# Optimization experiments

Measured on AMD Instinct MI355X. Metric: run time of the kernel, lower is better.

## Reference

```python
import jax, jax.numpy as jnp
import numpy as np

B, T, D_MODEL, STATE = 4, 4096, 1024, 256
LN_EPS = 1e-5


def setup_inputs() -> dict:
    key = jax.random.key(0)
    ks = jax.random.split(key, 8)
    x = jax.random.normal(ks[0], (B, T, D_MODEL), dtype=jnp.float32)
    bound_d = 1.0 / np.sqrt(D_MODEL)
    bound_n = 1.0 / np.sqrt(STATE)
    Wa_w = jax.random.normal(ks[1], (STATE, D_MODEL), dtype=jnp.float32) * 0.02
    Wa_b = jnp.zeros((STATE,), dtype=jnp.float32)
    WB_w = jax.random.normal(ks[2], (STATE, D_MODEL), dtype=jnp.float32) * 0.02
    WB_b = jax.random.uniform(ks[3], (STATE,), jnp.float32, -bound_d, bound_d)
    WC_w = jax.random.normal(ks[4], (D_MODEL, STATE), dtype=jnp.float32) * 0.02
    WC_b = jax.random.uniform(ks[5], (D_MODEL,), jnp.float32, -bound_n, bound_n)
    log_gamma = jnp.asarray(0.0, dtype=jnp.float32)
    D_skip = jax.random.normal(ks[6], (D_MODEL,), dtype=jnp.float32) * 0.01
    ln_w = jnp.ones((D_MODEL,), dtype=jnp.float32)
    ln_b = jnp.zeros((D_MODEL,), dtype=jnp.float32)
    return {"x": x, "Wa_w": Wa_w, "Wa_b": Wa_b, "log_gamma": log_gamma,
            "WB_w": WB_w, "WB_b": WB_b, "WC_w": WC_w, "WC_b": WC_b,
            "D_skip": D_skip, "ln_w": ln_w, "ln_b": ln_b}


def _layernorm(x, w, b):
    mu = jnp.mean(x, axis=-1, keepdims=True)
    var = jnp.mean(jnp.square(x - mu), axis=-1, keepdims=True)
    return (x - mu) * jax.lax.rsqrt(var + LN_EPS) * w + b


def reference(x, Wa_w, Wa_b, log_gamma, WB_w, WB_b, WC_w, WC_b, D_skip, ln_w, ln_b):
    residual = x
    xn = _layernorm(x, ln_w, ln_b)                      # (B,T,D)
    # Fourier eigenvalues: gamma * tanh(W_a x), FFT, magnitude-contracting scale
    gamma = jax.nn.sigmoid(log_gamma)
    a = gamma * jnp.tanh(jnp.einsum('btd,nd->btn', xn, Wa_w) + Wa_b)  # (B,T,n) real
    a_hat = jnp.fft.fft(a, axis=-1)                     # (B,T,n) complex, conj-symmetric
    mag = jnp.maximum(jnp.abs(a_hat), 1e-8)
    a_hat = a_hat * jax.nn.sigmoid(2.0 * (1.0 - mag))
    # Input projection in Fourier domain
    u = jnp.einsum('btd,nd->btn', xn, WB_w) + WB_b
    u_hat = jnp.fft.fft(u, axis=-1)                     # (B,T,n) complex
    # Linear recurrence h_t = a_t * h_{t-1} + b_t via associative scan over time
    def combine(c1, c2):
        a1, b1 = c1
        a2, b2 = c2
        return (a1 * a2, a2 * b1 + b2)
    _, h_hat = jax.lax.associative_scan(combine, (a_hat, u_hat), axis=1)
    h = jnp.real(jnp.fft.ifft(h_hat, axis=-1)).astype(x.dtype)        # (B,T,n)
    y = jnp.einsum('btn,dn->btd', h, WC_w) + WC_b + D_skip * residual
    return y
```

## Files before the change

### kernel.cpp

```cpp
#include <hip/hip_runtime.h>


typedef unsigned short ushort_t;
typedef short s16x8 __attribute__((ext_vector_type(8)));
typedef float f32x4 __attribute__((ext_vector_type(4)));
typedef _Float16 f16x8 __attribute__((ext_vector_type(8)));
typedef _Float16 f16x2 __attribute__((ext_vector_type(2)));

#define B_ 4
#define T_ 4096
#define D_ 1024
#define N_ 256
#define KB_ 129
#define M_ (B_*T_)

#define SWZ(i) ((i) ^ (((i) >> 3) & 6))
#define DR4(n) ((((n) & 3) << 6) | (((n) & 12) << 2) | (((n) & 48) >> 2) | (((n) >> 6) & 3))

__device__ __forceinline__ ushort_t f2bf(float f) {
  unsigned u = __float_as_uint(f);
  u = (u + 0x7FFFu + ((u >> 16) & 1u)) >> 16;
  return (ushort_t)u;
}
__device__ __forceinline__ float2 cmul(float2 a, float2 b) {
  return make_float2(a.x*b.x - a.y*b.y, a.x*b.y + a.y*b.x);
}
__device__ __forceinline__ float fast_tanh(float x) {
  return 1.f - 2.f / (__expf(2.f * x) + 1.f);
}

typedef const __attribute__((address_space(1))) unsigned glb_u32;
typedef __attribute__((address_space(3))) unsigned lds_u32;
__device__ __forceinline__ void gload16(const void* g, void* l) {
  __builtin_amdgcn_global_load_lds((glb_u32*)g, (lds_u32*)l, 16, 0, 0);
}

__global__ __launch_bounds__(256) void stats_prep_kernel(const float* __restrict__ x,
    float2* __restrict__ stats,
    const float* __restrict__ Wa, const float* __restrict__ WB,
    const float* __restrict__ WC, ushort_t* __restrict__ Wab,
    ushort_t* __restrict__ WCb) {
  int tid = threadIdx.x;
  if (blockIdx.x >= 4096) {
    int i4 = ((blockIdx.x - 4096) * 256 + tid) * 4;
    float4 v;
    ushort_t* dst;
    if (i4 < 262144)        { v = *(const float4*)(Wa + i4);          dst = Wab + i4; }
    else if (i4 < 524288)   { v = *(const float4*)(WB + i4 - 262144); dst = Wab + i4; }
    else                    { v = *(const float4*)(WC + i4 - 524288); dst = WCb + i4 - 524288; }
    ushort4 o;
    o.x = f2bf(v.x); o.y = f2bf(v.y); o.z = f2bf(v.z); o.w = f2bf(v.w);
    *(ushort4*)dst = o;
    return;
  }
  int lane = tid & 63, wv = tid >> 6;
  int row = blockIdx.x * 4 + wv;
  const float4* xr = (const float4*)(x + (size_t)row * D_);
  float s = 0.f, sq = 0.f;
  #pragma unroll
  for (int j = 0; j < 4; ++j) {
    float4 v = xr[lane + 64 * j];
    s  += v.x + v.y + v.z + v.w;
    sq += v.x*v.x + v.y*v.y + v.z*v.z + v.w*v.w;
  }
  #pragma unroll
  for (int off = 32; off >= 1; off >>= 1) {
    s  += __shfl_xor(s, off);
    sq += __shfl_xor(sq, off);
  }
  if (lane == 0) {
    float mu  = s * (1.0f / D_);
    float var = sq * (1.0f / D_) - mu * mu;
    stats[row] = make_float2(mu, rsqrtf(var + 1e-5f));
  }
}

__global__ __launch_bounds__(256) void gemm1_ln(
    const float* __restrict__ x, const float2* __restrict__ stats,
    const float* __restrict__ lnw, const float* __restrict__ lnb,
    const ushort_t* __restrict__ B, _Float16* __restrict__ C) {
  constexpr int NF = 2;
  __shared__ ushort_t Alds[128 * 64];
  __shared__ ushort_t Blds[64 * 64];
  int bid = blockIdx.x;
  int cpx = gridDim.x >> 3;
  bid = (bid & 7) * cpx + (bid >> 3);
  int mt = bid >> 3, nt = bid & 7;
  int m0 = mt * 128, n0 = nt * 64;
  int tid = threadIdx.x;
  int lane = tid & 63, wid = tid >> 6;
  int wm = wid >> 1, wn = wid & 1;

  int lr8 = lane >> 3;
  int gd  = (lane & 7) ^ lr8;
  const ushort_t* gB = B + (size_t)(n0 + wid * 16 + lr8) * D_ + gd * 8;
  ushort_t* lB = &Blds[(wid * 16) * 64];

  int rsub = tid >> 4, l16 = tid & 15;
  int slotA = ((l16 >> 1) ^ (rsub & 7)) * 8 + (l16 & 1) * 4;
  float2 st[8];
  #pragma unroll
  for (int it = 0; it < 8; ++it) st[it] = stats[m0 + rsub + it * 16];

  f32x4 acc[4][NF] = {};
  int rbase = lane & 15;
  int rb7 = lane & 7;
  int gk0 = lane >> 4;

  for (int k0 = 0; k0 < D_; k0 += 64) {
    __syncthreads();
    float4 wv = *(const float4*)(lnw + k0 + l16 * 4);
    float4 bv = *(const float4*)(lnb + k0 + l16 * 4);
    #pragma unroll
    for (int it = 0; it < 8; ++it) {
      int r = rsub + it * 16;
      float4 xv = *(const float4*)(x + (size_t)(m0 + r) * D_ + k0 + l16 * 4);
      float mu = st[it].x, rs = st[it].y;
      ushort4 o;
      o.x = f2bf((xv.x - mu) * rs * wv.x + bv.x);
      o.y = f2bf((xv.y - mu) * rs * wv.y + bv.y);
      o.z = f2bf((xv.z - mu) * rs * wv.z + bv.z);
      o.w = f2bf((xv.w - mu) * rs * wv.w + bv.w);
      *(ushort4*)(&Alds[r * 64 + slotA]) = o;
    }
    #pragma unroll
    for (int c = 0; c < 2; ++c)
      gload16(gB + (size_t)(c * 8) * D_ + k0, lB + c * 8 * 64);
    __syncthreads();
    #pragma unroll
    for (int kk = 0; kk < 2; ++kk) {
      int sl = ((gk0 + kk * 4) ^ rb7) * 8;
      s16x8 af[4], bf[NF];
      #pragma unroll
      for (int i = 0; i < 4; ++i)
        af[i] = *reinterpret_cast<const s16x8*>(&Alds[(wm * 64 + i * 16 + rbase) * 64 + sl]);
      #pragma unroll
      for (int j = 0; j < NF; ++j)
        bf[j] = *reinterpret_cast<const s16x8*>(&Blds[(wn * 32 + j * 16 + rbase) * 64 + sl]);
      #pragma unroll
      for (int i = 0; i < 4; ++i)
        #pragma unroll
        for (int j = 0; j < NF; ++j)
          acc[i][j] = __builtin_amdgcn_mfma_f32_16x16x32_bf16(af[i], bf[j], acc[i][j], 0, 0, 0);
    }
  }

  int r0 = (lane >> 4) * 4, cc = lane & 15;
  #pragma unroll
  for (int i = 0; i < 4; ++i)
    #pragma unroll
    for (int j = 0; j < NF; ++j) {
      int col = n0 + wn * 32 + j * 16 + cc;
      #pragma unroll
      for (int r = 0; r < 4; ++r) {
        int row = m0 + wm * 64 + i * 16 + r0 + r;
        C[(size_t)row * 512 + col] = (_Float16)acc[i][j][r];
      }
    }
}

__global__ __launch_bounds__(256) void gemm2_epi(
    const ushort_t* __restrict__ A, const ushort_t* __restrict__ B,
    float* __restrict__ C,
    const float* __restrict__ bias, const float* __restrict__ dskip,
    const float* __restrict__ xres) {
  constexpr int BN = 128, NF = 4;
  __shared__ ushort_t Alds[128 * 64];
  __shared__ ushort_t Blds[BN * 64];
  int bid = blockIdx.x;
  int cpx = gridDim.x >> 3;
  bid = (bid & 7) * cpx + (bid >> 3);
  int mt = bid >> 3, nt = bid & 7;
  int m0 = mt * 128, n0 = nt * BN;
  int tid = threadIdx.x;
  int lane = tid & 63, wid = tid >> 6;
  int wm = wid >> 1, wn = wid & 1;

  int lr8 = lane >> 3;
  int gd  = (lane & 7) ^ lr8;
  const ushort_t* gA = A + (size_t)(m0 + wid * 32 + lr8) * N_ + gd * 8;
  ushort_t* lA = &Alds[(wid * 32) * 64];
  const ushort_t* gB = B + (size_t)(n0 + wid * 32 + lr8) * N_ + gd * 8;
  ushort_t* lB = &Blds[(wid * 32) * 64];

  f32x4 acc[4][NF] = {};
  int rbase = lane & 15;
  int rb7 = lane & 7;
  int gk0 = lane >> 4;

  for (int k0 = 0; k0 < N_; k0 += 64) {
    __syncthreads();
    #pragma unroll
    for (int c = 0; c < 4; ++c) {
      gload16(gA + (size_t)(c * 8) * N_ + k0, lA + c * 8 * 64);
      gload16(gB + (size_t)(c * 8) * N_ + k0, lB + c * 8 * 64);
    }
    __syncthreads();
    #pragma unroll
    for (int kk = 0; kk < 2; ++kk) {
      int sl = ((gk0 + kk * 4) ^ rb7) * 8;
      s16x8 af[4], bf[NF];
      #pragma unroll
      for (int i = 0; i < 4; ++i)
        af[i] = *reinterpret_cast<const s16x8*>(&Alds[(wm * 64 + i * 16 + rbase) * 64 + sl]);
      #pragma unroll
      for (int j = 0; j < NF; ++j)
        bf[j] = *reinterpret_cast<const s16x8*>(&Blds[(wn * 64 + j * 16 + rbase) * 64 + sl]);
      #pragma unroll
      for (int i = 0; i < 4; ++i)
        #pragma unroll
        for (int j = 0; j < NF; ++j)
          acc[i][j] = __builtin_amdgcn_mfma_f32_16x16x32_bf16(af[i], bf[j], acc[i][j], 0, 0, 0);
    }
  }

  int r0 = (lane >> 4) * 4, cc = lane & 15;
  float bcol[NF], dcol[NF];
  #pragma unroll
  for (int j = 0; j < NF; ++j) {
    int col = n0 + wn * 64 + j * 16 + cc;
    bcol[j] = bias[col];
    dcol[j] = dskip[col];
  }
  #pragma unroll
  for (int i = 0; i < 4; ++i) {
    float xr[NF][4];
    #pragma unroll
    for (int j = 0; j < NF; ++j)
      #pragma unroll
      for (int r = 0; r < 4; ++r)
        xr[j][r] = xres[(size_t)(m0 + wm * 64 + i * 16 + r0 + r) * D_ +
                        n0 + wn * 64 + j * 16 + cc];
    #pragma unroll
    for (int j = 0; j < NF; ++j) {
      int col = n0 + wn * 64 + j * 16 + cc;
      #pragma unroll
      for (int r = 0; r < 4; ++r) {
        int row = m0 + wm * 64 + i * 16 + r0 + r;
        C[(size_t)row * D_ + col] = acc[i][j][r] + bcol[j] + dcol[j] * xr[j][r];
      }
    }
  }
}

__global__ __launch_bounds__(512) void fft_fwd(const _Float16* __restrict__ au,
    const float* __restrict__ ba, const float* __restrict__ bu,
    const float* __restrict__ lg, _Float16* __restrict__ ah, _Float16* __restrict__ uh) {
  __shared__ float2 Z[8][256];
  __shared__ float2 Tw[256];
  int tid = threadIdx.x;
  int m0 = blockIdx.x * 8;
  int tg = tid >> 6, lane = tid & 63;
  if (tid < 256) {
    float sn, cs;
    __sincosf(-6.2831853071795864f / 256.f * (float)tid, &sn, &cs);
    Tw[tid] = make_float2(cs, sn);
  }
  float gamma = 1.f / (1.f + __expf(-lg[0]));
  const _Float16* row = au + (size_t)(m0 + tg) * (2 * N_);
  #pragma unroll
  for (int j = 0; j < 4; ++j) {
    int n = lane + 64 * j;
    float a = gamma * fast_tanh((float)row[n] + ba[n]);
    float u = (float)row[N_ + n] + bu[n];
    Z[tg][SWZ(DR4(n))] = make_float2(a, u);
  }
  __syncthreads();
  #pragma unroll
  for (int ls = 0; ls < 4; ++ls) {
    const int Q = 1 << (2 * ls);
    const int step = 64 >> (2 * ls);
    int j = lane & (Q - 1);
    int g = lane >> (2 * ls);
    int base = g * (4 * Q) + j;
    float2 a0 = Z[tg][SWZ(base)];
    float2 a1 = Z[tg][SWZ(base + Q)];
    float2 a2 = Z[tg][SWZ(base + 2 * Q)];
    float2 a3 = Z[tg][SWZ(base + 3 * Q)];
    if (ls > 0) {
      int e = j * step;
      a1 = cmul(a1, Tw[e]);
      a2 = cmul(a2, Tw[2 * e]);
      a3 = cmul(a3, Tw[3 * e]);
    }
    float2 t0 = make_float2(a0.x + a2.x, a0.y + a2.y);
    float2 t1 = make_float2(a0.x - a2.x, a0.y - a2.y);
    float2 t2 = make_float2(a1.x + a3.x, a1.y + a3.y);
    float2 d  = make_float2(a1.x - a3.x, a1.y - a3.y);
    float2 t3 = make_float2(d.y, -d.x);
    Z[tg][SWZ(base)]         = make_float2(t0.x + t2.x, t0.y + t2.y);
    Z[tg][SWZ(base + Q)]     = make_float2(t1.x + t3.x, t1.y + t3.y);
    Z[tg][SWZ(base + 2 * Q)] = make_float2(t0.x - t2.x, t0.y - t2.y);
    Z[tg][SWZ(base + 3 * Q)] = make_float2(t1.x - t3.x, t1.y - t3.y);
  }
  __syncthreads();
  int b = m0 >> 12, tb = m0 & (T_ - 1);
  #pragma unroll
  for (int p = 0; p < 3; ++p) {
    int k = (tid >> 3) + p * 64;
    int tl = tid & 7;
    if (k <= 128) {
      float2 zk = Z[tl][SWZ(k)];
      float2 zn = Z[tl][SWZ((256 - k) & 255)];
      float2 Af = make_float2(0.5f * (zk.x + zn.x), 0.5f * (zk.y - zn.y));
      float2 Uf = make_float2(0.5f * (zk.y + zn.y), -0.5f * (zk.x - zn.x));
      float mag = fmaxf(sqrtf(Af.x * Af.x + Af.y * Af.y), 1e-8f);
      float scl = 1.f / (1.f + __expf(-2.f * (1.f - mag)));
      Af.x *= scl; Af.y *= scl;
      size_t off2 = (((size_t)(b * KB_ + k)) * T_ + tb + tl) * 2;
      f16x2 av; av[0] = (_Float16)Af.x; av[1] = (_Float16)Af.y;
      f16x2 uv; uv[0] = (_Float16)Uf.x; uv[1] = (_Float16)Uf.y;
      *(f16x2*)(ah + off2) = av;
      *(f16x2*)(uh + off2) = uv;
    }
  }
}

__global__ __launch_bounds__(512) void scan_kernel(const _Float16* __restrict__ ah,
                                                   _Float16* __restrict__ uh) {
  __shared__ float4 wagg[8];
  int tid = threadIdx.x;
  int lane = tid & 63, wv = tid >> 6;
  size_t base = (size_t)blockIdx.x * T_ * 2;
  const f16x8* a8 = (const f16x8*)(ah + base);
  f16x8* u8 = (f16x8*)(uh + base);
  f16x8 Av[2], Uv[2];
  #pragma unroll
  for (int q = 0; q < 2; ++q) { Av[q] = a8[tid * 2 + q]; Uv[q] = u8[tid * 2 + q]; }
  float2 La[8], Lb[8];
  float2 ra = make_float2(1.f, 0.f), rb = make_float2(0.f, 0.f);
  #pragma unroll
  for (int e = 0; e < 8; ++e) {
    const int q = e >> 2, i = (e & 3) * 2;
    float2 a = make_float2((float)Av[q][i], (float)Av[q][i + 1]);
    float2 u = make_float2((float)Uv[q][i], (float)Uv[q][i + 1]);
    float2 t = cmul(a, rb);
    rb = make_float2(t.x + u.x, t.y + u.y);
    ra = cmul(ra, a);
    La[e] = ra; Lb[e] = rb;
  }
  #pragma unroll
  for (int off = 1; off < 64; off <<= 1) {
    float ax = __shfl_up(ra.x, off, 64), ay = __shfl_up(ra.y, off, 64);
    float bx = __shfl_up(rb.x, off, 64), by = __shfl_up(rb.y, off, 64);
    if (lane >= off) {
      float2 Ap = make_float2(ax, ay), Bp = make_float2(bx, by);
      float2 nB = cmul(ra, Bp);
      nB.x += rb.x; nB.y += rb.y;
      ra = cmul(Ap, ra);
      rb = nB;
    }
  }
  if (lane == 63) wagg[wv] = make_float4(ra.x, ra.y, rb.x, rb.y);
  __syncthreads();
  float2 Bw = make_float2(0.f, 0.f);
  for (int w0 = 0; w0 < wv; ++w0) {
    float4 g = wagg[w0];
    float2 gA = make_float2(g.x, g.y), gB = make_float2(g.z, g.w);
    Bw = cmul(gA, Bw);
    Bw.x += gB.x; Bw.y += gB.y;
  }
  float ax = __shfl_up(ra.x, 1, 64), ay = __shfl_up(ra.y, 1, 64);
  float bx = __shfl_up(rb.x, 1, 64), by = __shfl_up(rb.y, 1, 64);
  float2 Ae, Be;
  if (lane == 0) { Ae = make_float2(1.f, 0.f); Be = make_float2(0.f, 0.f); }
  else           { Ae = make_float2(ax, ay);   Be = make_float2(bx, by);   }
  float2 Pb = cmul(Ae, Bw);
  Pb.x += Be.x; Pb.y += Be.y;
  #pragma unroll
  for (int q = 0; q < 2; ++q) {
    f16x8 o;
    #pragma unroll
    for (int e2 = 0; e2 < 4; ++e2) {
      const int e = q * 4 + e2;
      float2 h = cmul(La[e], Pb);
      h.x += Lb[e].x; h.y += Lb[e].y;
      o[e2 * 2]     = (_Float16)h.x;
      o[e2 * 2 + 1] = (_Float16)h.y;
    }
    u8[tid * 2 + q] = o;
  }
}

__global__ __launch_bounds__(256) void ifft_kernel(const _Float16* __restrict__ hh,
                                                   ushort_t* __restrict__ hb) {
  __shared__ float2 Hraw[8][132];
  __shared__ float2 Wz[4][256];
  __shared__ float2 Tw[256];
  int tid = threadIdx.x;
  int m0 = blockIdx.x * 8;
  int b = m0 >> 12, tb = m0 & (T_ - 1);
  {
    float sn, cs;
    __sincosf(6.2831853071795864f / 256.f * (float)tid, &sn, &cs);
    Tw[tid] = make_float2(cs, sn);
  }
  #pragma unroll
  for (int p = 0; p < 5; ++p) {
    int k = p * 32 + (tid >> 3), tl = tid & 7;
    if (k <= 128) {
      f16x2 hv = *(const f16x2*)(hh + (((size_t)(b * KB_ + k)) * T_ + tb + tl) * 2);
      Hraw[tl][k] = make_float2((float)hv[0], (float)hv[1]);
    }
  }
  __syncthreads();
  #pragma unroll
  for (int p = 0; p < 3; ++p) {
    int idx = p * 256 + tid;
    if (idx < 516) {
      int k = idx >> 2, pr = idx & 3;
      float2 h1 = Hraw[2 * pr][k], h2 = Hraw[2 * pr + 1][k];
      Wz[pr][SWZ(DR4(k))] = make_float2(h1.x - h2.y, h1.y + h2.x);
      if (k >= 1 && k <= 127)
        Wz[pr][SWZ(DR4(256 - k))] = make_float2(h1.x + h2.y, h2.x - h1.y);
    }
  }
  __syncthreads();
  int pr = tid >> 6, lane = tid & 63;
  #pragma unroll
  for (int ls = 0; ls < 4; ++ls) {
    const int Q = 1 << (2 * ls);
    const int step = 64 >> (2 * ls);
    int j = lane & (Q - 1);
    int g = lane >> (2 * ls);
    int base = g * (4 * Q) + j;
    float2 a0 = Wz[pr][SWZ(base)];
    float2 a1 = Wz[pr][SWZ(base + Q)];
    float2 a2 = Wz[pr][SWZ(base + 2 * Q)];
    float2 a3 = Wz[pr][SWZ(base + 3 * Q)];
    if (ls > 0) {
      int e = j * step;
      a1 = cmul(a1, Tw[e]);
      a2 = cmul(a2, Tw[2 * e]);
      a3 = cmul(a3, Tw[3 * e]);
    }
    float2 t0 = make_float2(a0.x + a2.x, a0.y + a2.y);
    float2 t1 = make_float2(a0.x - a2.x, a0.y - a2.y);
    float2 t2 = make_float2(a1.x + a3.x, a1.y + a3.y);
    float2 d  = make_float2(a1.x - a3.x, a1.y - a3.y);
    float2 t3 = make_float2(-d.y, d.x);
    Wz[pr][SWZ(base)]         = make_float2(t0.x + t2.x, t0.y + t2.y);
    Wz[pr][SWZ(base + Q)]     = make_float2(t1.x + t3.x, t1.y + t3.y);
    Wz[pr][SWZ(base + 2 * Q)] = make_float2(t0.x - t2.x, t0.y - t2.y);
    Wz[pr][SWZ(base + 3 * Q)] = make_float2(t1.x - t3.x, t1.y - t3.y);
  }
  const float inv = 1.f / 256.f;
  #pragma unroll
  for (int j = 0; j < 4; ++j) {
    int n = lane + 64 * j;
    float2 wv = Wz[pr][SWZ(n)];
    hb[(size_t)(m0 + 2 * pr) * N_ + n]     = f2bf(wv.x * inv);
    hb[(size_t)(m0 + 2 * pr + 1) * N_ + n] = f2bf(wv.y * inv);
  }
}

extern "C" void kernel_launch(void* const* d_in, const int* in_sizes, int n_in,
                              void* d_out, int out_size, void* d_ws, size_t ws_size,
                              hipStream_t stream) {
  const float* x      = (const float*)d_in[0];
  const float* Wa_w   = (const float*)d_in[1];
  const float* Wa_b   = (const float*)d_in[2];
  const float* lg     = (const float*)d_in[3];
  const float* WB_w   = (const float*)d_in[4];
  const float* WB_b   = (const float*)d_in[5];
  const float* WC_w   = (const float*)d_in[6];
  const float* WC_b   = (const float*)d_in[7];
  const float* D_skip = (const float*)d_in[8];
  const float* ln_w   = (const float*)d_in[9];
  const float* ln_b   = (const float*)d_in[10];
  float* out = (float*)d_out;
  char* ws = (char*)d_ws;

  float2*    stats = (float2*)(ws + 0);
  ushort_t*  Wab = (ushort_t*)(ws + 33554432);
  ushort_t*  WCb = (ushort_t*)(ws + 34603008);
  _Float16*  au  = (_Float16*)(ws + 35127296);
  ushort_t*  hb  = (ushort_t*)(ws + 35127296);
  _Float16*  ah  = (_Float16*)(ws + 0);
  _Float16*  uh  = (_Float16*)(ws + 16908288);

  stats_prep_kernel<<<4864, 256, 0, stream>>>(x, stats, Wa_w, WB_w, WC_w, Wab, WCb);
  gemm1_ln<<<1024, 256, 0, stream>>>(x, stats, ln_w, ln_b, Wab, au);
  fft_fwd<<<M_ / 8, 512, 0, stream>>>(au, Wa_b, WB_b, lg, ah, uh);
  scan_kernel<<<B_ * KB_, 512, 0, stream>>>(ah, uh);
  ifft_kernel<<<M_ / 8, 256, 0, stream>>>(uh, hb);
  gemm2_epi<<<1024, 256, 0, stream>>>(hb, WCb, out, WC_b, D_skip, x);
}
```

Measured before the change: 130.2 us.

## Materialize normalized bf16 activations in prep kernel and load GEMM A via LDS DMA

```diff
diff --git a/kernel.cpp b/kernel.cpp
--- a/kernel.cpp
+++ b/kernel.cpp
@@ -35,8 +35,9 @@
   __builtin_amdgcn_global_load_lds((glb_u32*)g, (lds_u32*)l, 16, 0, 0);
 }
 
-__global__ __launch_bounds__(256) void stats_prep_kernel(const float* __restrict__ x,
-    float2* __restrict__ stats,
+__global__ __launch_bounds__(256) void ln_prep_kernel(const float* __restrict__ x,
+    const float* __restrict__ w, const float* __restrict__ bb,
+    ushort_t* __restrict__ xn,
     const float* __restrict__ Wa, const float* __restrict__ WB,
     const float* __restrict__ WC, ushort_t* __restrict__ Wab,
     ushort_t* __restrict__ WCb) {
@@ -56,29 +57,41 @@
   int lane = tid & 63, wv = tid >> 6;
   int row = blockIdx.x * 4 + wv;
   const float4* xr = (const float4*)(x + (size_t)row * D_);
+  float4 v[4];
   float s = 0.f, sq = 0.f;
   #pragma unroll
   for (int j = 0; j < 4; ++j) {
-    float4 v = xr[lane + 64 * j];
-    s  += v.x + v.y + v.z + v.w;
-    sq += v.x*v.x + v.y*v.y + v.z*v.z + v.w*v.w;
+    v[j] = xr[lane + 64 * j];
+    s  += v[j].x + v[j].y + v[j].z + v[j].w;
+    sq += v[j].x*v[j].x + v[j].y*v[j].y + v[j].z*v[j].z + v[j].w*v[j].w;
   }
   #pragma unroll
   for (int off = 32; off >= 1; off >>= 1) {
     s  += __shfl_xor(s, off);
     sq += __shfl_xor(sq, off);
   }
-  if (lane == 0) {
-    float mu  = s * (1.0f / D_);
-    float var = sq * (1.0f / D_) - mu * mu;
-    stats[row] = make_float2(mu, rsqrtf(var + 1e-5f));
-  }
-}
-
-__global__ __launch_bounds__(256) void gemm1_ln(
-    const float* __restrict__ x, const float2* __restrict__ stats,
-    const float* __restrict__ lnw, const float* __restrict__ lnb,
-    const ushort_t* __restrict__ B, _Float16* __restrict__ C) {
+  float mu  = s * (1.0f / D_);
+  float var = sq * (1.0f / D_) - mu * mu;
+  float rs  = rsqrtf(var + 1e-5f);
+  const float4* w4 = (const float4*)w;
+  const float4* b4 = (const float4*)bb;
+  ushort4* o4 = (ushort4*)(xn + (size_t)row * D_);
+  #pragma unroll
+  for (int j = 0; j < 4; ++j) {
+    float4 wv_ = w4[lane + 64 * j];
+    float4 bv_ = b4[lane + 64 * j];
+    ushort4 o;
+    o.x = f2bf((v[j].x - mu) * rs * wv_.x + bv_.x);
+    o.y = f2bf((v[j].y - mu) * rs * wv_.y + bv_.y);
+    o.z = f2bf((v[j].z - mu) * rs * wv_.z + bv_.z);
+    o.w = f2bf((v[j].w - mu) * rs * wv_.w + bv_.w);
+    o4[lane + 64 * j] = o;
+  }
+}
+
+__global__ __launch_bounds__(256) void gemm1_k(
+    const ushort_t* __restrict__ A, const ushort_t* __restrict__ B,
+    _Float16* __restrict__ C) {
   constexpr int NF = 2;
   __shared__ ushort_t Alds[128 * 64];
   __shared__ ushort_t Blds[64 * 64];
@@ -93,14 +106,10 @@
 
   int lr8 = lane >> 3;
   int gd  = (lane & 7) ^ lr8;
+  const ushort_t* gA = A + (size_t)(m0 + wid * 32 + lr8) * D_ + gd * 8;
+  ushort_t* lA = &Alds[(wid * 32) * 64];
   const ushort_t* gB = B + (size_t)(n0 + wid * 16 + lr8) * D_ + gd * 8;
   ushort_t* lB = &Blds[(wid * 16) * 64];
-
-  int rsub = tid >> 4, l16 = tid & 15;
-  int slotA = ((l16 >> 1) ^ (rsub & 7)) * 8 + (l16 & 1) * 4;
-  float2 st[8];
-  #pragma unroll
-  for (int it = 0; it < 8; ++it) st[it] = stats[m0 + rsub + it * 16];
 
   f32x4 acc[4][NF] = {};
   int rbase = lane & 15;
@@ -109,20 +118,9 @@
 
   for (int k0 = 0; k0 < D_; k0 += 64) {
     __syncthreads();
-    float4 wv = *(const float4*)(lnw + k0 + l16 * 4);
-    float4 bv = *(const float4*)(lnb + k0 + l16 * 4);
-    #pragma unroll
-    for (int it = 0; it < 8; ++it) {
-      int r = rsub + it * 16;
-      float4 xv = *(const float4*)(x + (size_t)(m0 + r) * D_ + k0 + l16 * 4);
-      float mu = st[it].x, rs = st[it].y;
-      ushort4 o;
-      o.x = f2bf((xv.x - mu) * rs * wv.x + bv.x);
-      o.y = f2bf((xv.y - mu) * rs * wv.y + bv.y);
-      o.z = f2bf((xv.z - mu) * rs * wv.z + bv.z);
-      o.w = f2bf((xv.w - mu) * rs * wv.w + bv.w);
-      *(ushort4*)(&Alds[r * 64 + slotA]) = o;
-    }
+    #pragma unroll
+    for (int c = 0; c < 4; ++c)
+      gload16(gA + (size_t)(c * 8) * D_ + k0, lA + c * 8 * 64);
     #pragma unroll
     for (int c = 0; c < 2; ++c)
       gload16(gB + (size_t)(c * 8) * D_ + k0, lB + c * 8 * 64);
@@ -471,7 +469,7 @@
   float* out = (float*)d_out;
   char* ws = (char*)d_ws;
 
-  float2*    stats = (float2*)(ws + 0);
+  ushort_t*  xn  = (ushort_t*)(ws + 0);
   ushort_t*  Wab = (ushort_t*)(ws + 33554432);
   ushort_t*  WCb = (ushort_t*)(ws + 34603008);
   _Float16*  au  = (_Float16*)(ws + 35127296);
@@ -479,8 +477,9 @@
   _Float16*  ah  = (_Float16*)(ws + 0);
   _Float16*  uh  = (_Float16*)(ws + 16908288);
 
-  stats_prep_kernel<<<4864, 256, 0, stream>>>(x, stats, Wa_w, WB_w, WC_w, Wab, WCb);
-  gemm1_ln<<<1024, 256, 0, stream>>>(x, stats, ln_w, ln_b, Wab, au);
+  ln_prep_kernel<<<4864, 256, 0, stream>>>(x, ln_w, ln_b, xn,
+                                           Wa_w, WB_w, WC_w, Wab, WCb);
+  gemm1_k<<<1024, 256, 0, stream>>>(xn, Wab, au);
   fft_fwd<<<M_ / 8, 512, 0, stream>>>(au, Wa_b, WB_b, lg, ah, uh);
   scan_kernel<<<B_ * KB_, 512, 0, stream>>>(ah, uh);
   ifft_kernel<<<M_ / 8, 256, 0, stream>>>(uh, hb);
```

New measurement: 104.3 us (median of 2 runs). -19.9%, faster.
